# Kernel optimization log

Measured on AMD Instinct MI355X. Metric: run time of the kernel, lower is better.

## Reference

```python
import jax, jax.numpy as jnp
import numpy as np

G, NP, K, H, DH, D, NL = 256, 1000, 8, 8, 10, 80, 10  # graphs, nodes/graph, knn, heads, d_head, hidden, layers


def setup_inputs() -> dict:
    key = jax.random.key(0)
    ks = jax.random.split(key, 16)
    rn = lambda k, shape: (jax.random.normal(k, shape, jnp.float32) * 0.05)
    return dict(
        h_feat=jax.random.normal(ks[0], (G, NP, 9), jnp.float32),
        bn_gamma=jnp.ones((9,), jnp.float32), bn_beta=jnp.zeros((9,), jnp.float32),
        W_emb=rn(ks[1], (9, D)), b_emb=jnp.zeros((D,), jnp.float32),
        Wq=rn(ks[2], (NL, D, D)), Wk=rn(ks[3], (NL, D, D)), Wv=rn(ks[4], (NL, D, D)),
        Wo=rn(ks[5], (NL, D, D)), bo=jnp.zeros((NL, D), jnp.float32),
        W1=rn(ks[6], (NL, D, 2 * D)), b1=jnp.zeros((NL, 2 * D), jnp.float32),
        W2=rn(ks[7], (NL, 2 * D, D)), b2=jnp.zeros((NL, D), jnp.float32),
        Wr0=rn(ks[8], (D, 40)), br0=jnp.zeros((40,), jnp.float32),
        Wr1=rn(ks[9], (40, 20)), br1=jnp.zeros((20,), jnp.float32),
        Wr2=rn(ks[10], (20, 64)), br2=jnp.zeros((64,), jnp.float32),
        W_clust=rn(ks[11], (64, 3)),
        W_beta=rn(ks[12], (64, 1)), b_beta=jnp.zeros((1,), jnp.float32),
    )


def _forward(h_feat, bn_gamma, bn_beta, W_emb, b_emb, Wq, Wk, Wv, Wo, bo,
             W1, b1, W2, b2, Wr0, br0, Wr1, br1, Wr2, br2, W_clust, W_beta, b_beta):
    # knn graph on raw coords (first 3 feature columns), per graph, k=8 (self included)
    coords = h_feat[..., :3]
    d2 = jnp.sum((coords[:, :, None, :] - coords[:, None, :, :]) ** 2, -1)  # [G,NP,NP]
    nbr = jax.lax.top_k(-d2, K)[1]  # [G,NP,K] neighbor indices per destination node
    gidx = jnp.arange(G)[:, None, None]

    # BatchNorm1d (training-mode batch stats over all nodes) + embedding
    x = h_feat.reshape(-1, 9)
    mu = x.mean(0)
    var = x.var(0)
    x = (x - mu) / jnp.sqrt(var + 1e-5) * bn_gamma + bn_beta
    h = (x @ W_emb + b_emb).reshape(G, NP, D)

    inv_sqrt_d = jnp.float32(1.0 / np.sqrt(DH))

    def layer(h, p):
        wq, wk, wv, wo, bo_, w1, b1_, w2, b2_ = p
        q = (h @ wq).reshape(G, NP, H, DH)
        k_ = (h @ wk).reshape(G, NP, H, DH)
        v = (h @ wv).reshape(G, NP, H, DH)
        kn = k_[gidx, nbr]  # [G,NP,K,H,DH] gather src K over edges
        vn = v[gidx, nbr]
        s = jnp.einsum('gnkhd,gnhd->gnkh', kn, q) * inv_sqrt_d
        s = jnp.exp(jnp.clip(s, -5.0, 5.0))  # scaled_exp with clamp
        wV = jnp.einsum('gnkh,gnkhd->gnhd', s, vn)
        attn = (wV / (s.sum(2)[..., None] + 1e-6)).reshape(G, NP, D)
        h = h + attn @ wo + bo_  # O proj + residual (no LN/BN)
        h = h + jax.nn.relu(h @ w1 + b1_) @ w2 + b2_  # FFN + residual
        return h, None

    h, _ = jax.lax.scan(layer, h, (Wq, Wk, Wv, Wo, bo, W1, b1, W2, b2))

    # MLPReadout 80->40->20->64 (ReLU between), then clustering coords + beta
    y = h.reshape(-1, D)
    y = jax.nn.relu(y @ Wr0 + br0)
    y = jax.nn.relu(y @ Wr1 + br1)
    y = y @ Wr2 + br2
    cc = y @ W_clust  # [N,3], no bias
    beta = y @ W_beta + b_beta  # [N,1]
    return jnp.concatenate([cc, beta], axis=1)  # [N,4]


def reference(h_feat, bn_gamma, bn_beta, W_emb, b_emb, Wq, Wk, Wv, Wo, bo,
              W1, b1, W2, b2, Wr0, br0, Wr1, br1, Wr2, br2, W_clust, W_beta, b_beta):
    return _forward(h_feat, bn_gamma, bn_beta, W_emb, b_emb, Wq, Wk, Wv, Wo, bo,
                    W1, b1, W2, b2, Wr0, br0, Wr1, br1, Wr2, br2, W_clust, W_beta, b_beta)
```

## Files before the change

### kernel.cpp

```cpp
#include <hip/hip_runtime.h>
#include <cstdint>
#include <cstddef>


typedef __attribute__((ext_vector_type(8))) short short8v;
typedef __attribute__((ext_vector_type(4))) float f32x4;

#define MFMA16(ACC, A, B) ACC = __builtin_amdgcn_mfma_f32_16x16x32_bf16(A, B, ACC, 0, 0, 0)
#define MF3(ACC, AH, AL, BH, BL) { MFMA16(ACC, AH, BH); MFMA16(ACC, AH, BL); MFMA16(ACC, AL, BH); }

__device__ __forceinline__ void splitbf(float x, unsigned short& hi, unsigned short& lo) {
  unsigned u = __float_as_uint(x);
  unsigned r = u + 0x7FFFu + ((u >> 16) & 1u);
  hi = (unsigned short)(r >> 16);
  float hf = __uint_as_float(((unsigned)hi) << 16);
  float lf = x - hf;
  unsigned u2 = __float_as_uint(lf);
  unsigned r2 = u2 + 0x7FFFu + ((u2 >> 16) & 1u);
  lo = (unsigned short)(r2 >> 16);
}

__global__ __launch_bounds__(256) void knn_kernel(const float* __restrict__ hf, int* __restrict__ nbr) {
  __shared__ float cs[3000];
  int b = blockIdx.x;
  int g = b >> 2;
  int q = b & 3;
  for (int i = threadIdx.x; i < 3000; i += 256) {
    cs[i] = hf[((size_t)g * 1000 + (i / 3)) * 9 + (i % 3)];
  }
  __syncthreads();
  int tid = threadIdx.x;
  if (tid < 250) {
    int n = q * 250 + tid;
    float cx = cs[n * 3 + 0], cy = cs[n * 3 + 1], cz = cs[n * 3 + 2];
    float bd[8];
    int bi[8];
    #pragma unroll
    for (int q2 = 0; q2 < 8; ++q2) { bd[q2] = 3.402823466e38f; bi[q2] = 0; }
    for (int j = 0; j < 1000; ++j) {
      float dx = __fsub_rn(cx, cs[j * 3 + 0]);
      float dy = __fsub_rn(cy, cs[j * 3 + 1]);
      float dz = __fsub_rn(cz, cs[j * 3 + 2]);
      float d2 = __fadd_rn(__fadd_rn(__fmul_rn(dx, dx), __fmul_rn(dy, dy)), __fmul_rn(dz, dz));
      if (d2 < bd[7]) {
        bd[7] = d2; bi[7] = j;
        #pragma unroll
        for (int q2 = 7; q2 >= 1; --q2) {
          if (bd[q2] < bd[q2 - 1]) {
            float tf = bd[q2]; bd[q2] = bd[q2 - 1]; bd[q2 - 1] = tf;
            int ti = bi[q2]; bi[q2] = bi[q2 - 1]; bi[q2 - 1] = ti;
          }
        }
      }
    }
    #pragma unroll
    for (int kk = 0; kk < 8; ++kk) nbr[((size_t)g * 1000 + n) * 8 + kk] = bi[kk];
  }
}

__global__ __launch_bounds__(256) void bn_stat1(const float* __restrict__ hf, float* __restrict__ partial) {
  __shared__ float red[4][18];
  int row = blockIdx.x * 256 + threadIdx.x;
  float s[9], ss[9];
  #pragma unroll
  for (int f = 0; f < 9; ++f) {
    float v = hf[(size_t)row * 9 + f];
    s[f] = v;
    ss[f] = v * v;
  }
  for (int off = 32; off > 0; off >>= 1) {
    #pragma unroll
    for (int f = 0; f < 9; ++f) {
      s[f] += __shfl_down(s[f], off);
      ss[f] += __shfl_down(ss[f], off);
    }
  }
  int wid = threadIdx.x >> 6, lane = threadIdx.x & 63;
  if (lane == 0) {
    #pragma unroll
    for (int f = 0; f < 9; ++f) { red[wid][f] = s[f]; red[wid][9 + f] = ss[f]; }
  }
  __syncthreads();
  if (threadIdx.x < 18) {
    partial[(size_t)blockIdx.x * 18 + threadIdx.x] =
        red[0][threadIdx.x] + red[1][threadIdx.x] + red[2][threadIdx.x] + red[3][threadIdx.x];
  }
}

__global__ __launch_bounds__(256) void bn_stat2(const float* __restrict__ partial, float* __restrict__ stats) {
  __shared__ double sd[9][28], qd[9][28];
  int tid = threadIdx.x;
  if (tid < 252) {
    int f = tid % 9, gq = tid / 9;
    double s = 0.0, q = 0.0;
    for (int b = gq; b < 1000; b += 28) {
      s += (double)partial[b * 18 + f];
      q += (double)partial[b * 18 + 9 + f];
    }
    sd[f][gq] = s;
    qd[f][gq] = q;
  }
  __syncthreads();
  if (tid < 9) {
    double s = 0.0, q = 0.0;
    for (int g2 = 0; g2 < 28; ++g2) { s += sd[tid][g2]; q += qd[tid][g2]; }
    double mu = s / 256000.0;
    double var = q / 256000.0 - mu * mu;
    stats[tid] = (float)mu;
    stats[9 + tid] = (float)(1.0 / sqrt(var + 1e-5));
  }
}

__global__ __launch_bounds__(256) void split_tr(const float* __restrict__ src, unsigned short* __restrict__ dhi,
                                                unsigned short* __restrict__ dlo, int R, int C, int KS) {
  const float* s = src + (size_t)blockIdx.x * R * C;
  unsigned short* dh = dhi + (size_t)blockIdx.x * C * KS;
  unsigned short* dl = dlo + (size_t)blockIdx.x * C * KS;
  int n = C * KS;
  for (int i = threadIdx.x; i < n; i += 256) {
    int c = i / KS, kk = i % KS;
    float v = (kk < R) ? s[kk * C + c] : 0.f;
    unsigned short h, l;
    splitbf(v, h, l);
    dh[i] = h;
    dl[i] = l;
  }
}

__global__ __launch_bounds__(320) void embed_kernel(const float* __restrict__ hf, const float* __restrict__ stats,
                                                    const float* __restrict__ gamma, const float* __restrict__ beta,
                                                    const float* __restrict__ We, const float* __restrict__ be,
                                                    float* __restrict__ h) {
  __shared__ __align__(16) float xs[40 * 9];
  size_t p0 = (size_t)blockIdx.x * 40;
  for (int i = threadIdx.x; i < 360; i += 320) {
    int f = i % 9;
    float x = hf[p0 * 9 + i];
    xs[i] = (x - stats[f]) * stats[9 + f] * gamma[f] + beta[f];
  }
  __syncthreads();
  int c = threadIdx.x % 80, pg = threadIdx.x / 80;
  float we[9];
  #pragma unroll
  for (int f = 0; f < 9; ++f) we[f] = We[f * 80 + c];
  float bias = be[c];
  for (int pp = 0; pp < 10; ++pp) {
    int p = pg * 10 + pp;
    float acc = 0.f;
    #pragma unroll
    for (int f = 0; f < 9; ++f) acc = fmaf(xs[p * 9 + f], we[f], acc);
    h[(p0 + p) * 80 + c] = acc + bias;
  }
}

__global__ __launch_bounds__(320) void kv_kernel(const float* __restrict__ h,
                                                 const unsigned short* __restrict__ WkH, const unsigned short* __restrict__ WkL,
                                                 const unsigned short* __restrict__ WvH, const unsigned short* __restrict__ WvL,
                                                 float* __restrict__ kb, float* __restrict__ vb) {
  __shared__ __align__(16) unsigned short ahi[48 * 104];
  __shared__ __align__(16) unsigned short alo[48 * 104];
  size_t p0 = (size_t)blockIdx.x * 40;
  int tid = threadIdx.x;
  int lane = tid & 63, wv = tid >> 6;
  int fr = lane & 15, fq = lane >> 4;
  for (int i = tid; i < 800; i += 320) {
    int row = i / 20, kq = i % 20;
    float4 v = reinterpret_cast<const float4*>(h + (p0 + row) * 80)[kq];
    unsigned short h0, l0, h1, l1, h2, l2, h3, l3;
    splitbf(v.x, h0, l0); splitbf(v.y, h1, l1); splitbf(v.z, h2, l2); splitbf(v.w, h3, l3);
    int off = row * 104 + kq * 4;
    *reinterpret_cast<unsigned*>(&ahi[off]) = (unsigned)h0 | ((unsigned)h1 << 16);
    *reinterpret_cast<unsigned*>(&ahi[off + 2]) = (unsigned)h2 | ((unsigned)h3 << 16);
    *reinterpret_cast<unsigned*>(&alo[off]) = (unsigned)l0 | ((unsigned)l1 << 16);
    *reinterpret_cast<unsigned*>(&alo[off + 2]) = (unsigned)l2 | ((unsigned)l3 << 16);
  }
  for (int i = tid; i < 384; i += 320) {
    int row = i >> 3, kk = 80 + ((i & 7) << 1);
    int off = row * 104 + kk;
    *reinterpret_cast<unsigned*>(&ahi[off]) = 0u;
    *reinterpret_cast<unsigned*>(&alo[off]) = 0u;
  }
  __syncthreads();
  int bcol = wv * 16 + fr;
  f32x4 ck0 = {0.f, 0.f, 0.f, 0.f}, ck1 = ck0, ck2 = ck0;
  f32x4 cv0 = ck0, cv1 = ck0, cv2 = ck0;
  #pragma unroll
  for (int ks = 0; ks < 3; ++ks) {
    int boff = bcol * 96 + ks * 32 + fq * 8;
    short8v bkh = *reinterpret_cast<const short8v*>(WkH + boff);
    short8v bkl = *reinterpret_cast<const short8v*>(WkL + boff);
    short8v bvh = *reinterpret_cast<const short8v*>(WvH + boff);
    short8v bvl = *reinterpret_cast<const short8v*>(WvL + boff);
    int a0 = (0 * 16 + fr) * 104 + ks * 32 + fq * 8;
    int a1 = (1 * 16 + fr) * 104 + ks * 32 + fq * 8;
    int a2 = (2 * 16 + fr) * 104 + ks * 32 + fq * 8;
    short8v ah0 = *reinterpret_cast<const short8v*>(ahi + a0);
    short8v al0 = *reinterpret_cast<const short8v*>(alo + a0);
    MF3(ck0, ah0, al0, bkh, bkl); MF3(cv0, ah0, al0, bvh, bvl);
    short8v ah1 = *reinterpret_cast<const short8v*>(ahi + a1);
    short8v al1 = *reinterpret_cast<const short8v*>(alo + a1);
    MF3(ck1, ah1, al1, bkh, bkl); MF3(cv1, ah1, al1, bvh, bvl);
    short8v ah2 = *reinterpret_cast<const short8v*>(ahi + a2);
    short8v al2 = *reinterpret_cast<const short8v*>(alo + a2);
    MF3(ck2, ah2, al2, bkh, bkl); MF3(cv2, ah2, al2, bvh, bvl);
  }
  #pragma unroll
  for (int j = 0; j < 4; ++j) {
    int r0 = fq * 4 + j;
    kb[(p0 + r0) * 80 + bcol] = ck0[j];
    vb[(p0 + r0) * 80 + bcol] = cv0[j];
    int r1 = 16 + r0;
    kb[(p0 + r1) * 80 + bcol] = ck1[j];
    vb[(p0 + r1) * 80 + bcol] = cv1[j];
    int r2 = 32 + r0;
    if (r2 < 40) {
      kb[(p0 + r2) * 80 + bcol] = ck2[j];
      vb[(p0 + r2) * 80 + bcol] = cv2[j];
    }
  }
}

__global__ __launch_bounds__(320) void battn_kernel(const float* __restrict__ h, const float* __restrict__ kb,
                                                    const float* __restrict__ vb, const int* __restrict__ nbr,
                                                    const unsigned short* __restrict__ WqH, const unsigned short* __restrict__ WqL,
                                                    const unsigned short* __restrict__ WoH, const unsigned short* __restrict__ WoL,
                                                    const float* __restrict__ bo,
                                                    const unsigned short* __restrict__ W1H, const unsigned short* __restrict__ W1L,
                                                    const float* __restrict__ b1,
                                                    const unsigned short* __restrict__ W2H, const unsigned short* __restrict__ W2L,
                                                    const float* __restrict__ b2, float* __restrict__ hout) {
  __shared__ __align__(16) unsigned short ahi[48 * 168];
  __shared__ __align__(16) unsigned short alo[48 * 168];
  __shared__ __align__(16) float qa[40 * 84];
  int b = blockIdx.x;
  int xcd = b & 7;
  int r = b >> 3;
  int graph = (xcd << 5) + (r / 25);
  int jb = r % 25;
  size_t gbase = (size_t)graph * 1000;
  size_t pbase = gbase + (size_t)jb * 40;
  int tid = threadIdx.x;
  int lane = tid & 63, wv = tid >> 6;
  int fr = lane & 15, fq = lane >> 4;
  int pA = tid >> 3, hhA = tid & 7;
  int nb[8];
  #pragma unroll
  for (int kk = 0; kk < 8; ++kk) nb[kk] = nbr[(pbase + pA) * 8 + kk];
  for (int i = tid; i < 800; i += 320) {
    int row = i / 20, kq = i % 20;
    float4 v = reinterpret_cast<const float4*>(h + (pbase + row) * 80)[kq];
    unsigned short h0, l0, h1, l1, h2_, l2, h3, l3;
    splitbf(v.x, h0, l0); splitbf(v.y, h1, l1); splitbf(v.z, h2_, l2); splitbf(v.w, h3, l3);
    int off = row * 168 + kq * 4;
    *reinterpret_cast<unsigned*>(&ahi[off]) = (unsigned)h0 | ((unsigned)h1 << 16);
    *reinterpret_cast<unsigned*>(&ahi[off + 2]) = (unsigned)h2_ | ((unsigned)h3 << 16);
    *reinterpret_cast<unsigned*>(&alo[off]) = (unsigned)l0 | ((unsigned)l1 << 16);
    *reinterpret_cast<unsigned*>(&alo[off + 2]) = (unsigned)l2 | ((unsigned)l3 << 16);
  }
  for (int i = tid; i < 384; i += 320) {
    int row = i >> 3, kk = 80 + ((i & 7) << 1);
    int off = row * 168 + kk;
    *reinterpret_cast<unsigned*>(&ahi[off]) = 0u;
    *reinterpret_cast<unsigned*>(&alo[off]) = 0u;
  }
  __syncthreads();
  int bcol = wv * 16 + fr;
  {
    f32x4 c0 = {0.f, 0.f, 0.f, 0.f}, c1 = c0, c2 = c0;
    #pragma unroll
    for (int ks = 0; ks < 3; ++ks) {
      int boff = bcol * 96 + ks * 32 + fq * 8;
      short8v bh = *reinterpret_cast<const short8v*>(WqH + boff);
      short8v bl = *reinterpret_cast<const short8v*>(WqL + boff);
      int a0 = (0 * 16 + fr) * 168 + ks * 32 + fq * 8;
      int a1 = (1 * 16 + fr) * 168 + ks * 32 + fq * 8;
      int a2 = (2 * 16 + fr) * 168 + ks * 32 + fq * 8;
      short8v ah0 = *reinterpret_cast<const short8v*>(ahi + a0);
      short8v al0 = *reinterpret_cast<const short8v*>(alo + a0);
      MF3(c0, ah0, al0, bh, bl);
      short8v ah1 = *reinterpret_cast<const short8v*>(ahi + a1);
      short8v al1 = *reinterpret_cast<const short8v*>(alo + a1);
      MF3(c1, ah1, al1, bh, bl);
      short8v ah2 = *reinterpret_cast<const short8v*>(ahi + a2);
      short8v al2 = *reinterpret_cast<const short8v*>(alo + a2);
      MF3(c2, ah2, al2, bh, bl);
    }
    #pragma unroll
    for (int j = 0; j < 4; ++j) {
      int r0 = fq * 4 + j;
      qa[r0 * 84 + bcol] = c0[j];
      qa[(16 + r0) * 84 + bcol] = c1[j];
      int r2 = 32 + r0;
      if (r2 < 40) qa[r2 * 84 + bcol] = c2[j];
    }
  }
  __syncthreads();
  {
    int p = pA, hh = hhA;
    float qv[10];
    #pragma unroll
    for (int d = 0; d < 10; ++d) qv[d] = qa[p * 84 + hh * 10 + d];
    float sv[8];
    float denom = 0.f;
    #pragma unroll
    for (int kk = 0; kk < 8; ++kk) {
      const float2* kr = reinterpret_cast<const float2*>(kb + (gbase + nb[kk]) * 80 + hh * 10);
      float acc = 0.f;
      #pragma unroll
      for (int d2 = 0; d2 < 5; ++d2) {
        float2 kv2 = kr[d2];
        acc = fmaf(qv[2 * d2], kv2.x, acc);
        acc = fmaf(qv[2 * d2 + 1], kv2.y, acc);
      }
      float s = acc * 0.31622776601683794f;
      s = fminf(fmaxf(s, -5.f), 5.f);
      s = expf(s);
      sv[kk] = s;
      denom += s;
    }
    float wV[10] = {0, 0, 0, 0, 0, 0, 0, 0, 0, 0};
    #pragma unroll
    for (int kk = 0; kk < 8; ++kk) {
      const float2* vr = reinterpret_cast<const float2*>(vb + (gbase + nb[kk]) * 80 + hh * 10);
      #pragma unroll
      for (int d2 = 0; d2 < 5; ++d2) {
        float2 vv = vr[d2];
        wV[2 * d2] = fmaf(sv[kk], vv.x, wV[2 * d2]);
        wV[2 * d2 + 1] = fmaf(sv[kk], vv.y, wV[2 * d2 + 1]);
      }
    }
    float dn = denom + 1e-6f;
    #pragma unroll
    for (int d2 = 0; d2 < 5; ++d2) {
      float x0 = wV[2 * d2] / dn;
      float x1 = wV[2 * d2 + 1] / dn;
      unsigned short h0, l0, h1, l1;
      splitbf(x0, h0, l0); splitbf(x1, h1, l1);
      int off = p * 168 + hh * 10 + 2 * d2;
      *reinterpret_cast<unsigned*>(&ahi[off]) = (unsigned)h0 | ((unsigned)h1 << 16);
      *reinterpret_cast<unsigned*>(&alo[off]) = (unsigned)l0 | ((unsigned)l1 << 16);
    }
  }
  __syncthreads();
  f32x4 o0 = {0.f, 0.f, 0.f, 0.f}, o1 = o0, o2 = o0;
  {
    #pragma unroll
    for (int ks = 0; ks < 3; ++ks) {
      int boff = bcol * 96 + ks * 32 + fq * 8;
      short8v bh = *reinterpret_cast<const short8v*>(WoH + boff);
      short8v bl = *reinterpret_cast<const short8v*>(WoL + boff);
      int a0 = (0 * 16 + fr) * 168 + ks * 32 + fq * 8;
      int a1 = (1 * 16 + fr) * 168 + ks * 32 + fq * 8;
      int a2 = (2 * 16 + fr) * 168 + ks * 32 + fq * 8;
      short8v ah0 = *reinterpret_cast<const short8v*>(ahi + a0);
      short8v al0 = *reinterpret_cast<const short8v*>(alo + a0);
      MF3(o0, ah0, al0, bh, bl);
      short8v ah1 = *reinterpret_cast<const short8v*>(ahi + a1);
      short8v al1 = *reinterpret_cast<const short8v*>(alo + a1);
      MF3(o1, ah1, al1, bh, bl);
      short8v ah2 = *reinterpret_cast<const short8v*>(ahi + a2);
      short8v al2 = *reinterpret_cast<const short8v*>(alo + a2);
      MF3(o2, ah2, al2, bh, bl);
    }
  }
  __syncthreads();
  {
    float bias = bo[bcol];
    #pragma unroll
    for (int j = 0; j < 4; ++j) {
      int r0 = fq * 4 + j;
      float h2v = h[(pbase + r0) * 80 + bcol] + o0[j] + bias;
      qa[r0 * 84 + bcol] = h2v;
      unsigned short hh_, ll_;
      splitbf(h2v, hh_, ll_);
      ahi[r0 * 168 + bcol] = hh_;
      alo[r0 * 168 + bcol] = ll_;
      int r1 = 16 + r0;
      h2v = h[(pbase + r1) * 80 + bcol] + o1[j] + bias;
      qa[r1 * 84 + bcol] = h2v;
      splitbf(h2v, hh_, ll_);
      ahi[r1 * 168 + bcol] = hh_;
      alo[r1 * 168 + bcol] = ll_;
      int r2 = 32 + r0;
      if (r2 < 40) {
        h2v = h[(pbase + r2) * 80 + bcol] + o2[j] + bias;
        qa[r2 * 84 + bcol] = h2v;
        splitbf(h2v, hh_, ll_);
        ahi[r2 * 168 + bcol] = hh_;
        alo[r2 * 168 + bcol] = ll_;
      }
    }
  }
  __syncthreads();
  f32x4 t00 = {0.f, 0.f, 0.f, 0.f}, t01 = t00, t02 = t00;
  f32x4 t10 = t00, t11 = t00, t12 = t00;
  {
    int bc0 = wv * 16 + fr, bc1 = (wv + 5) * 16 + fr;
    #pragma unroll
    for (int ks = 0; ks < 3; ++ks) {
      int b0 = bc0 * 96 + ks * 32 + fq * 8;
      int b1o = bc1 * 96 + ks * 32 + fq * 8;
      short8v bh0 = *reinterpret_cast<const short8v*>(W1H + b0);
      short8v bl0 = *reinterpret_cast<const short8v*>(W1L + b0);
      short8v bh1 = *reinterpret_cast<const short8v*>(W1H + b1o);
      short8v bl1 = *reinterpret_cast<const short8v*>(W1L + b1o);
      int a0 = (0 * 16 + fr) * 168 + ks * 32 + fq * 8;
      int a1 = (1 * 16 + fr) * 168 + ks * 32 + fq * 8;
      int a2 = (2 * 16 + fr) * 168 + ks * 32 + fq * 8;
      short8v ah0 = *reinterpret_cast<const short8v*>(ahi + a0);
      short8v al0 = *reinterpret_cast<const short8v*>(alo + a0);
      MF3(t00, ah0, al0, bh0, bl0); MF3(t10, ah0, al0, bh1, bl1);
      short8v ah1 = *reinterpret_cast<const short8v*>(ahi + a1);
      short8v al1 = *reinterpret_cast<const short8v*>(alo + a1);
      MF3(t01, ah1, al1, bh0, bl0); MF3(t11, ah1, al1, bh1, bl1);
      short8v ah2 = *reinterpret_cast<const short8v*>(ahi + a2);
      short8v al2 = *reinterpret_cast<const short8v*>(alo + a2);
      MF3(t02, ah2, al2, bh0, bl0); MF3(t12, ah2, al2, bh1, bl1);
    }
  }
  __syncthreads();
  {
    int bc0 = wv * 16 + fr, bc1 = (wv + 5) * 16 + fr;
    float bias0 = b1[bc0], bias1 = b1[bc1];
    #pragma unroll
    for (int j = 0; j < 4; ++j) {
      unsigned short hh_, ll_;
      int r0 = fq * 4 + j;
      float t = fmaxf(t00[j] + bias0, 0.f);
      splitbf(t, hh_, ll_); ahi[r0 * 168 + bc0] = hh_; alo[r0 * 168 + bc0] = ll_;
      t = fmaxf(t10[j] + bias1, 0.f);
      splitbf(t, hh_, ll_); ahi[r0 * 168 + bc1] = hh_; alo[r0 * 168 + bc1] = ll_;
      int r1 = 16 + r0;
      t = fmaxf(t01[j] + bias0, 0.f);
      splitbf(t, hh_, ll_); ahi[r1 * 168 + bc0] = hh_; alo[r1 * 168 + bc0] = ll_;
      t = fmaxf(t11[j] + bias1, 0.f);
      splitbf(t, hh_, ll_); ahi[r1 * 168 + bc1] = hh_; alo[r1 * 168 + bc1] = ll_;
      int r2 = 32 + r0;
      if (r2 < 40) {
        t = fmaxf(t02[j] + bias0, 0.f);
        splitbf(t, hh_, ll_); ahi[r2 * 168 + bc0] = hh_; alo[r2 * 168 + bc0] = ll_;
        t = fmaxf(t12[j] + bias1, 0.f);
        splitbf(t, hh_, ll_); ahi[r2 * 168 + bc1] = hh_; alo[r2 * 168 + bc1] = ll_;
      }
    }
  }
  __syncthreads();
  {
    f32x4 c0 = {0.f, 0.f, 0.f, 0.f}, c1 = c0, c2 = c0;
    #pragma unroll
    for (int ks = 0; ks < 5; ++ks) {
      int boff = bcol * 160 + ks * 32 + fq * 8;
      short8v bh = *reinterpret_cast<const short8v*>(W2H + boff);
      short8v bl = *reinterpret_cast<const short8v*>(W2L + boff);
      int a0 = (0 * 16 + fr) * 168 + ks * 32 + fq * 8;
      int a1 = (1 * 16 + fr) * 168 + ks * 32 + fq * 8;
      int a2 = (2 * 16 + fr) * 168 + ks * 32 + fq * 8;
      short8v ah0 = *reinterpret_cast<const short8v*>(ahi + a0);
      short8v al0 = *reinterpret_cast<const short8v*>(alo + a0);
      MF3(c0, ah0, al0, bh, bl);
      short8v ah1 = *reinterpret_cast<const short8v*>(ahi + a1);
      short8v al1 = *reinterpret_cast<const short8v*>(alo + a1);
      MF3(c1, ah1, al1, bh, bl);
      short8v ah2 = *reinterpret_cast<const short8v*>(ahi + a2);
      short8v al2 = *reinterpret_cast<const short8v*>(alo + a2);
      MF3(c2, ah2, al2, bh, bl);
    }
    float bias = b2[bcol];
    #pragma unroll
    for (int j = 0; j < 4; ++j) {
      int r0 = fq * 4 + j;
      hout[(pbase + r0) * 80 + bcol] = qa[r0 * 84 + bcol] + c0[j] + bias;
      int r1 = 16 + r0;
      hout[(pbase + r1) * 80 + bcol] = qa[r1 * 84 + bcol] + c1[j] + bias;
      int r2 = 32 + r0;
      if (r2 < 40) hout[(pbase + r2) * 80 + bcol] = qa[r2 * 84 + bcol] + c2[j] + bias;
    }
  }
}

__global__ __launch_bounds__(320) void readout_kernel(const float* __restrict__ h, const float* __restrict__ Wr0,
                                                      const float* __restrict__ br0, const float* __restrict__ Wr1,
                                                      const float* __restrict__ br1, const float* __restrict__ Wr2,
                                                      const float* __restrict__ br2, const float* __restrict__ Wc,
                                                      const float* __restrict__ Wb, const float* __restrict__ bb,
                                                      float* __restrict__ out) {
  __shared__ __align__(16) float hs[3200];
  __shared__ __align__(16) float y0s[40 * 40];
  __shared__ __align__(16) float y1s[40 * 20];
  __shared__ __align__(16) float y2s[40 * 64];
  size_t p0 = (size_t)blockIdx.x * 40;
  int tid = threadIdx.x;
  {
    const float4* src = reinterpret_cast<const float4*>(h + p0 * 80);
    float4* dst = reinterpret_cast<float4*>(hs);
    for (int i = tid; i < 800; i += 320) dst[i] = src[i];
  }
  __syncthreads();
  {
    int c = tid % 40, grp = tid / 40;
    if (grp < 5) {
      float wcol[80];
      #pragma unroll
      for (int kk = 0; kk < 80; ++kk) wcol[kk] = Wr0[kk * 40 + c];
      float bias = br0[c];
      float acc[8] = {};
      #pragma unroll
      for (int j = 0; j < 8; ++j) {
        const float4* r4 = reinterpret_cast<const float4*>(hs + (grp * 8 + j) * 80);
        #pragma unroll
        for (int kq = 0; kq < 20; ++kq) {
          float4 hv = r4[kq];
          acc[j] = fmaf(hv.x, wcol[4 * kq + 0], acc[j]);
          acc[j] = fmaf(hv.y, wcol[4 * kq + 1], acc[j]);
          acc[j] = fmaf(hv.z, wcol[4 * kq + 2], acc[j]);
          acc[j] = fmaf(hv.w, wcol[4 * kq + 3], acc[j]);
        }
      }
      #pragma unroll
      for (int j = 0; j < 8; ++j) y0s[(grp * 8 + j) * 40 + c] = fmaxf(acc[j] + bias, 0.f);
    }
  }
  __syncthreads();
  {
    int c = tid % 20, grp = tid / 20;
    if (grp < 5) {
      float wcol[40];
      #pragma unroll
      for (int kk = 0; kk < 40; ++kk) wcol[kk] = Wr1[kk * 20 + c];
      float bias = br1[c];
      float acc[8] = {};
      #pragma unroll
      for (int j = 0; j < 8; ++j) {
        const float4* r4 = reinterpret_cast<const float4*>(y0s + (grp * 8 + j) * 40);
        #pragma unroll
        for (int kq = 0; kq < 10; ++kq) {
          float4 hv = r4[kq];
          acc[j] = fmaf(hv.x, wcol[4 * kq + 0], acc[j]);
          acc[j] = fmaf(hv.y, wcol[4 * kq + 1], acc[j]);
          acc[j] = fmaf(hv.z, wcol[4 * kq + 2], acc[j]);
          acc[j] = fmaf(hv.w, wcol[4 * kq + 3], acc[j]);
        }
      }
      #pragma unroll
      for (int j = 0; j < 8; ++j) y1s[(grp * 8 + j) * 20 + c] = fmaxf(acc[j] + bias, 0.f);
    }
  }
  __syncthreads();
  {
    int c = tid % 64, grp = tid / 64;
    float wcol[20];
    #pragma unroll
    for (int kk = 0; kk < 20; ++kk) wcol[kk] = Wr2[kk * 64 + c];
    float bias = br2[c];
    float acc[8] = {};
    #pragma unroll
    for (int j = 0; j < 8; ++j) {
      const float4* r4 = reinterpret_cast<const float4*>(y1s + (grp * 8 + j) * 20);
      #pragma unroll
      for (int kq = 0; kq < 5; ++kq) {
        float4 hv = r4[kq];
        acc[j] = fmaf(hv.x, wcol[4 * kq + 0], acc[j]);
        acc[j] = fmaf(hv.y, wcol[4 * kq + 1], acc[j]);
        acc[j] = fmaf(hv.z, wcol[4 * kq + 2], acc[j]);
        acc[j] = fmaf(hv.w, wcol[4 * kq + 3], acc[j]);
      }
    }
    #pragma unroll
    for (int j = 0; j < 8; ++j) y2s[(grp * 8 + j) * 64 + c] = acc[j] + bias;
  }
  __syncthreads();
  {
    int c = tid % 4, p = tid / 4;
    if (p < 40) {
      float wcol[64];
      if (c < 3) {
        #pragma unroll
        for (int kk = 0; kk < 64; ++kk) wcol[kk] = Wc[kk * 3 + c];
      } else {
        #pragma unroll
        for (int kk = 0; kk < 64; ++kk) wcol[kk] = Wb[kk];
      }
      float acc = 0.f;
      #pragma unroll
      for (int kk = 0; kk < 64; ++kk) acc = fmaf(y2s[p * 64 + kk], wcol[kk], acc);
      if (c == 3) acc += bb[0];
      out[(p0 + p) * 4 + c] = acc;
    }
  }
}

extern "C" void kernel_launch(void* const* d_in, const int* in_sizes, int n_in,
                              void* d_out, int out_size, void* d_ws, size_t ws_size,
                              hipStream_t stream) {
  const float* hf = (const float*)d_in[0];
  const float* gamma = (const float*)d_in[1];
  const float* beta = (const float*)d_in[2];
  const float* We = (const float*)d_in[3];
  const float* be = (const float*)d_in[4];
  const float* Wq = (const float*)d_in[5];
  const float* Wk = (const float*)d_in[6];
  const float* Wv = (const float*)d_in[7];
  const float* Wo = (const float*)d_in[8];
  const float* bo = (const float*)d_in[9];
  const float* W1 = (const float*)d_in[10];
  const float* b1 = (const float*)d_in[11];
  const float* W2 = (const float*)d_in[12];
  const float* b2 = (const float*)d_in[13];
  const float* Wr0 = (const float*)d_in[14];
  const float* br0 = (const float*)d_in[15];
  const float* Wr1 = (const float*)d_in[16];
  const float* br1 = (const float*)d_in[17];
  const float* Wr2 = (const float*)d_in[18];
  const float* br2 = (const float*)d_in[19];
  const float* Wc = (const float*)d_in[20];
  const float* Wb = (const float*)d_in[21];
  const float* bb = (const float*)d_in[22];
  float* out = (float*)d_out;

  char* wsp = (char*)d_ws;
  int* nbr = (int*)wsp;            wsp += (size_t)256000 * 8 * 4;
  float* hA = (float*)wsp;         wsp += (size_t)256000 * 80 * 4;
  float* kbuf = (float*)wsp;       wsp += (size_t)256000 * 80 * 4;
  float* vbuf = (float*)wsp;       wsp += (size_t)256000 * 80 * 4;
  float* partial = (float*)wsp;    wsp += (size_t)1000 * 18 * 4;
  float* stats = (float*)wsp;      wsp += 128;
  unsigned short* WqH = (unsigned short*)wsp; wsp += (size_t)10 * 7680 * 2;
  unsigned short* WqL = (unsigned short*)wsp; wsp += (size_t)10 * 7680 * 2;
  unsigned short* WkH = (unsigned short*)wsp; wsp += (size_t)10 * 7680 * 2;
  unsigned short* WkL = (unsigned short*)wsp; wsp += (size_t)10 * 7680 * 2;
  unsigned short* WvH = (unsigned short*)wsp; wsp += (size_t)10 * 7680 * 2;
  unsigned short* WvL = (unsigned short*)wsp; wsp += (size_t)10 * 7680 * 2;
  unsigned short* WoH = (unsigned short*)wsp; wsp += (size_t)10 * 7680 * 2;
  unsigned short* WoL = (unsigned short*)wsp; wsp += (size_t)10 * 7680 * 2;
  unsigned short* W1H = (unsigned short*)wsp; wsp += (size_t)10 * 15360 * 2;
  unsigned short* W1L = (unsigned short*)wsp; wsp += (size_t)10 * 15360 * 2;
  unsigned short* W2H = (unsigned short*)wsp; wsp += (size_t)10 * 12800 * 2;
  unsigned short* W2L = (unsigned short*)wsp; wsp += (size_t)10 * 12800 * 2;

  knn_kernel<<<1024, 256, 0, stream>>>(hf, nbr);
  bn_stat1<<<1000, 256, 0, stream>>>(hf, partial);
  bn_stat2<<<1, 256, 0, stream>>>(partial, stats);
  split_tr<<<10, 256, 0, stream>>>(Wq, WqH, WqL, 80, 80, 96);
  split_tr<<<10, 256, 0, stream>>>(Wk, WkH, WkL, 80, 80, 96);
  split_tr<<<10, 256, 0, stream>>>(Wv, WvH, WvL, 80, 80, 96);
  split_tr<<<10, 256, 0, stream>>>(Wo, WoH, WoL, 80, 80, 96);
  split_tr<<<10, 256, 0, stream>>>(W1, W1H, W1L, 80, 160, 96);
  split_tr<<<10, 256, 0, stream>>>(W2, W2H, W2L, 160, 80, 160);
  embed_kernel<<<6400, 320, 0, stream>>>(hf, stats, gamma, beta, We, be, hA);
  for (int l = 0; l < 10; ++l) {
    kv_kernel<<<6400, 320, 0, stream>>>(hA, WkH + (size_t)l * 7680, WkL + (size_t)l * 7680,
                                        WvH + (size_t)l * 7680, WvL + (size_t)l * 7680, kbuf, vbuf);
    battn_kernel<<<6400, 320, 0, stream>>>(hA, kbuf, vbuf, nbr,
                                           WqH + (size_t)l * 7680, WqL + (size_t)l * 7680,
                                           WoH + (size_t)l * 7680, WoL + (size_t)l * 7680, bo + (size_t)l * 80,
                                           W1H + (size_t)l * 15360, W1L + (size_t)l * 15360, b1 + (size_t)l * 160,
                                           W2H + (size_t)l * 12800, W2L + (size_t)l * 12800, b2 + (size_t)l * 80, hA);
  }
  readout_kernel<<<6400, 320, 0, stream>>>(hA, Wr0, br0, Wr1, br1, Wr2, br2, Wc, Wb, bb, out);
}
```

Baseline: 3.554 ms.

## Drop attention shared q buffer and vectorize KNN coordinate loads with smaller blocks

The fused attention kernel no longer keeps a separate fp32 shared array for q and the residual. q is now stored as split bf16 hi/lo pairs in the existing ahi/alo staging buffers, and the post-attention residual stays in registers. This cuts shared memory per block, which could allow more blocks per CU. The cost is an extra barrier and a small precision loss from rebuilding q out of the hi+lo pair. Separately, the KNN kernel switches to 128-thread blocks over a doubled grid and reads coordinates from shared memory with float4 loads, four candidates per iteration.

```diff
diff --git a/kernel.cpp b/kernel.cpp
--- a/kernel.cpp
+++ b/kernel.cpp
@@ -20,35 +20,59 @@
   lo = (unsigned short)(r2 >> 16);
 }
 
-__global__ __launch_bounds__(256) void knn_kernel(const float* __restrict__ hf, int* __restrict__ nbr) {
-  __shared__ float cs[3000];
+__device__ __forceinline__ float bf2f(unsigned short v) {
+  return __uint_as_float(((unsigned)v) << 16);
+}
+
+__global__ __launch_bounds__(128) void knn_kernel(const float* __restrict__ hf, int* __restrict__ nbr) {
+  __shared__ __align__(16) float cs[3000];
   int b = blockIdx.x;
-  int g = b >> 2;
-  int q = b & 3;
-  for (int i = threadIdx.x; i < 3000; i += 256) {
+  int g = b >> 3;
+  int q = b & 7;
+  for (int i = threadIdx.x; i < 3000; i += 128) {
     cs[i] = hf[((size_t)g * 1000 + (i / 3)) * 9 + (i % 3)];
   }
   __syncthreads();
   int tid = threadIdx.x;
-  if (tid < 250) {
-    int n = q * 250 + tid;
+  if (tid < 125) {
+    int n = q * 125 + tid;
     float cx = cs[n * 3 + 0], cy = cs[n * 3 + 1], cz = cs[n * 3 + 2];
     float bd[8];
     int bi[8];
     #pragma unroll
     for (int q2 = 0; q2 < 8; ++q2) { bd[q2] = 3.402823466e38f; bi[q2] = 0; }
-    for (int j = 0; j < 1000; ++j) {
-      float dx = __fsub_rn(cx, cs[j * 3 + 0]);
-      float dy = __fsub_rn(cy, cs[j * 3 + 1]);
-      float dz = __fsub_rn(cz, cs[j * 3 + 2]);
-      float d2 = __fadd_rn(__fadd_rn(__fmul_rn(dx, dx), __fmul_rn(dy, dy)), __fmul_rn(dz, dz));
-      if (d2 < bd[7]) {
-        bd[7] = d2; bi[7] = j;
-        #pragma unroll
-        for (int q2 = 7; q2 >= 1; --q2) {
-          if (bd[q2] < bd[q2 - 1]) {
-            float tf = bd[q2]; bd[q2] = bd[q2 - 1]; bd[q2 - 1] = tf;
-            int ti = bi[q2]; bi[q2] = bi[q2 - 1]; bi[q2 - 1] = ti;
+    for (int j = 0; j < 1000; j += 4) {
+      float4 a = *reinterpret_cast<const float4*>(cs + j * 3);
+      float4 b4 = *reinterpret_cast<const float4*>(cs + j * 3 + 4);
+      float4 c4 = *reinterpret_cast<const float4*>(cs + j * 3 + 8);
+      float d2v[4];
+      {
+        float dx = __fsub_rn(cx, a.x), dy = __fsub_rn(cy, a.y), dz = __fsub_rn(cz, a.z);
+        d2v[0] = __fadd_rn(__fadd_rn(__fmul_rn(dx, dx), __fmul_rn(dy, dy)), __fmul_rn(dz, dz));
+      }
+      {
+        float dx = __fsub_rn(cx, a.w), dy = __fsub_rn(cy, b4.x), dz = __fsub_rn(cz, b4.y);
+        d2v[1] = __fadd_rn(__fadd_rn(__fmul_rn(dx, dx), __fmul_rn(dy, dy)), __fmul_rn(dz, dz));
+      }
+      {
+        float dx = __fsub_rn(cx, b4.z), dy = __fsub_rn(cy, b4.w), dz = __fsub_rn(cz, c4.x);
+        d2v[2] = __fadd_rn(__fadd_rn(__fmul_rn(dx, dx), __fmul_rn(dy, dy)), __fmul_rn(dz, dz));
+      }
+      {
+        float dx = __fsub_rn(cx, c4.y), dy = __fsub_rn(cy, c4.z), dz = __fsub_rn(cz, c4.w);
+        d2v[3] = __fadd_rn(__fadd_rn(__fmul_rn(dx, dx), __fmul_rn(dy, dy)), __fmul_rn(dz, dz));
+      }
+      #pragma unroll
+      for (int u = 0; u < 4; ++u) {
+        float d2 = d2v[u];
+        if (d2 < bd[7]) {
+          bd[7] = d2; bi[7] = j + u;
+          #pragma unroll
+          for (int q2 = 7; q2 >= 1; --q2) {
+            if (bd[q2] < bd[q2 - 1]) {
+              float tf = bd[q2]; bd[q2] = bd[q2 - 1]; bd[q2 - 1] = tf;
+              int ti = bi[q2]; bi[q2] = bi[q2 - 1]; bi[q2 - 1] = ti;
+            }
           }
         }
       }
@@ -231,7 +255,6 @@
                                                     const float* __restrict__ b2, float* __restrict__ hout) {
   __shared__ __align__(16) unsigned short ahi[48 * 168];
   __shared__ __align__(16) unsigned short alo[48 * 168];
-  __shared__ __align__(16) float qa[40 * 84];
   int b = blockIdx.x;
   int xcd = b & 7;
   int r = b >> 3;
@@ -265,8 +288,8 @@
   }
   __syncthreads();
   int bcol = wv * 16 + fr;
-  {
-    f32x4 c0 = {0.f, 0.f, 0.f, 0.f}, c1 = c0, c2 = c0;
+  f32x4 q0 = {0.f, 0.f, 0.f, 0.f}, q1 = q0, q2 = q0;
+  {
     #pragma unroll
     for (int ks = 0; ks < 3; ++ks) {
       int boff = bcol * 96 + ks * 32 + fq * 8;
@@ -277,21 +300,31 @@
       int a2 = (2 * 16 + fr) * 168 + ks * 32 + fq * 8;
       short8v ah0 = *reinterpret_cast<const short8v*>(ahi + a0);
       short8v al0 = *reinterpret_cast<const short8v*>(alo + a0);
-      MF3(c0, ah0, al0, bh, bl);
+      MF3(q0, ah0, al0, bh, bl);
       short8v ah1 = *reinterpret_cast<const short8v*>(ahi + a1);
       short8v al1 = *reinterpret_cast<const short8v*>(alo + a1);
-      MF3(c1, ah1, al1, bh, bl);
+      MF3(q1, ah1, al1, bh, bl);
       short8v ah2 = *reinterpret_cast<const short8v*>(ahi + a2);
       short8v al2 = *reinterpret_cast<const short8v*>(alo + a2);
-      MF3(c2, ah2, al2, bh, bl);
-    }
+      MF3(q2, ah2, al2, bh, bl);
+    }
+  }
+  __syncthreads();
+  {
     #pragma unroll
     for (int j = 0; j < 4; ++j) {
+      unsigned short hh_, ll_;
       int r0 = fq * 4 + j;
-      qa[r0 * 84 + bcol] = c0[j];
-      qa[(16 + r0) * 84 + bcol] = c1[j];
+      splitbf(q0[j], hh_, ll_);
+      ahi[r0 * 168 + bcol] = hh_; alo[r0 * 168 + bcol] = ll_;
+      int r1 = 16 + r0;
+      splitbf(q1[j], hh_, ll_);
+      ahi[r1 * 168 + bcol] = hh_; alo[r1 * 168 + bcol] = ll_;
       int r2 = 32 + r0;
-      if (r2 < 40) qa[r2 * 84 + bcol] = c2[j];
+      if (r2 < 40) {
+        splitbf(q2[j], hh_, ll_);
+        ahi[r2 * 168 + bcol] = hh_; alo[r2 * 168 + bcol] = ll_;
+      }
     }
   }
   __syncthreads();
@@ -299,7 +332,13 @@
     int p = pA, hh = hhA;
     float qv[10];
     #pragma unroll
-    for (int d = 0; d < 10; ++d) qv[d] = qa[p * 84 + hh * 10 + d];
+    for (int d2 = 0; d2 < 5; ++d2) {
+      int off = p * 168 + hh * 10 + 2 * d2;
+      unsigned uh = *reinterpret_cast<const unsigned*>(&ahi[off]);
+      unsigned ul = *reinterpret_cast<const unsigned*>(&alo[off]);
+      qv[2 * d2] = bf2f((unsigned short)uh) + bf2f((unsigned short)ul);
+      qv[2 * d2 + 1] = bf2f((unsigned short)(uh >> 16)) + bf2f((unsigned short)(ul >> 16));
+    }
     float sv[8];
     float denom = 0.f;
     #pragma unroll
@@ -368,26 +407,20 @@
     float bias = bo[bcol];
     #pragma unroll
     for (int j = 0; j < 4; ++j) {
+      unsigned short hh_, ll_;
       int r0 = fq * 4 + j;
-      float h2v = h[(pbase + r0) * 80 + bcol] + o0[j] + bias;
-      qa[r0 * 84 + bcol] = h2v;
-      unsigned short hh_, ll_;
-      splitbf(h2v, hh_, ll_);
-      ahi[r0 * 168 + bcol] = hh_;
-      alo[r0 * 168 + bcol] = ll_;
+      o0[j] = h[(pbase + r0) * 80 + bcol] + o0[j] + bias;
+      splitbf(o0[j], hh_, ll_);
+      ahi[r0 * 168 + bcol] = hh_; alo[r0 * 168 + bcol] = ll_;
       int r1 = 16 + r0;
-      h2v = h[(pbase + r1) * 80 + bcol] + o1[j] + bias;
-      qa[r1 * 84 + bcol] = h2v;
-      splitbf(h2v, hh_, ll_);
-      ahi[r1 * 168 + bcol] = hh_;
-      alo[r1 * 168 + bcol] = ll_;
+      o1[j] = h[(pbase + r1) * 80 + bcol] + o1[j] + bias;
+      splitbf(o1[j], hh_, ll_);
+      ahi[r1 * 168 + bcol] = hh_; alo[r1 * 168 + bcol] = ll_;
       int r2 = 32 + r0;
       if (r2 < 40) {
-        h2v = h[(pbase + r2) * 80 + bcol] + o2[j] + bias;
-        qa[r2 * 84 + bcol] = h2v;
-        splitbf(h2v, hh_, ll_);
-        ahi[r2 * 168 + bcol] = hh_;
-        alo[r2 * 168 + bcol] = ll_;
+        o2[j] = h[(pbase + r2) * 80 + bcol] + o2[j] + bias;
+        splitbf(o2[j], hh_, ll_);
+        ahi[r2 * 168 + bcol] = hh_; alo[r2 * 168 + bcol] = ll_;
       }
     }
   }
@@ -469,11 +502,11 @@
     #pragma unroll
     for (int j = 0; j < 4; ++j) {
       int r0 = fq * 4 + j;
-      hout[(pbase + r0) * 80 + bcol] = qa[r0 * 84 + bcol] + c0[j] + bias;
+      hout[(pbase + r0) * 80 + bcol] = o0[j] + c0[j] + bias;
       int r1 = 16 + r0;
-      hout[(pbase + r1) * 80 + bcol] = qa[r1 * 84 + bcol] + c1[j] + bias;
+      hout[(pbase + r1) * 80 + bcol] = o1[j] + c1[j] + bias;
       int r2 = 32 + r0;
-      if (r2 < 40) hout[(pbase + r2) * 80 + bcol] = qa[r2 * 84 + bcol] + c2[j] + bias;
+      if (r2 < 40) hout[(pbase + r2) * 80 + bcol] = o2[j] + c2[j] + bias;
     }
   }
 }
@@ -637,7 +670,7 @@
   unsigned short* W2H = (unsigned short*)wsp; wsp += (size_t)10 * 12800 * 2;
   unsigned short* W2L = (unsigned short*)wsp; wsp += (size_t)10 * 12800 * 2;
 
-  knn_kernel<<<1024, 256, 0, stream>>>(hf, nbr);
+  knn_kernel<<<2048, 128, 0, stream>>>(hf, nbr);
   bn_stat1<<<1000, 256, 0, stream>>>(hf, partial);
   bn_stat2<<<1, 256, 0, stream>>>(partial, stats);
   split_tr<<<10, 256, 0, stream>>>(Wq, WqH, WqL, 80, 80, 96);
```

New measurement: 3.568 ms. About the same (+0.4%).
